# Optimization experiments

Measured on AMD Instinct MI355X. Metric: run time of the kernel, lower is better.

The kernel has to match this reference:

```python
import jax, jax.numpy as jnp
import numpy as np

M1 = M2 = M3 = 6  # retained Fourier modes per axis (matches init_kwargs)
TWO_PI = 2.0 * np.pi


def _freq_grid(kx, ky, kz):
    KX, KY, KZ = jnp.meshgrid(kx, ky, kz, indexing='ij')
    return jnp.stack([KX.ravel(), KY.ravel(), KZ.ravel()], axis=-1)  # [M, 3]


def _cplx(w):
    return w[..., 0] + 1j * w[..., 1]


def setup_inputs() -> dict:
    key = jax.random.key(0)
    k1, k2, k3, k4, k5, k6 = jax.random.split(key, 6)
    B, C, N = 2, 32, 8192
    scale = 1.0 / (C * C)
    return {
        'x': jax.random.normal(k1, (B, C, N), dtype=jnp.float32),
        'pos': jax.random.uniform(k2, (B, N, 3), dtype=jnp.float32),
        'w1': scale * jax.random.uniform(k3, (C, C, M1, M2, M3, 2), dtype=jnp.float32),
        'w2': scale * jax.random.uniform(k4, (C, C, M1, M2, M3, 2), dtype=jnp.float32),
        'w3': scale * jax.random.uniform(k5, (C, C, M1, M2, M3, 2), dtype=jnp.float32),
        'w4': scale * jax.random.uniform(k6, (C, C, M1, M2, M3, 2), dtype=jnp.float32),
    }


def reference(x, pos, w1, w2, w3, w4):
    m1, m2, m3 = M1, M2, M3
    B, C, N = x.shape
    # FFT-ordered frequencies: [0..m-1, -m..-1]
    kx = jnp.concatenate([jnp.arange(m1), jnp.arange(-m1, 0)]).astype(jnp.float32)
    ky = jnp.concatenate([jnp.arange(m2), jnp.arange(-m2, 0)]).astype(jnp.float32)
    kz_full = jnp.concatenate([jnp.arange(m3), jnp.arange(-m3, 0)]).astype(jnp.float32)
    kz_half = jnp.arange(m3).astype(jnp.float32)
    Kf = _freq_grid(kx, ky, kz_full)                     # [M, 3], M = 2m1*2m2*2m3
    Kh = _freq_grid(kx, ky, kz_half)                     # [Mh, 3], Mh = 2m1*2m2*m3
    Ki = jnp.concatenate([Kh, -Kh[::-1]], axis=0)        # [2Mh, 3] Hermitian extension

    # Nonuniform forward Fourier transform (transformer.forward), fused with permutes:
    V_fwd = jnp.exp(-1j * TWO_PI * jnp.einsum('md,bnd->bmn', Kf, pos))  # [B, M, N]
    x_ft = jnp.einsum('bmn,bcn->bcm', V_fwd, x.astype(jnp.complex64))   # [B, C, M]
    x_ft = x_ft.reshape(B, C, 2 * m1, 2 * m2, 2 * m3)

    def mul(a, w):
        return jnp.einsum('bixyz,ioxyz->boxyz', a, _cplx(w))

    out = jnp.zeros((B, C, 2 * m1, 2 * m2, m3), dtype=jnp.complex64)
    out = out.at[:, :, :m1, :m2, :].set(mul(x_ft[:, :, :m1, :m2, :m3], w1))
    out = out.at[:, :, m1:, :m2, :].set(mul(x_ft[:, :, m1:, :m2, :m3], w2))
    out = out.at[:, :, :m1, m2:, :].set(mul(x_ft[:, :, :m1, m2:, :m3], w3))
    out = out.at[:, :, m1:, m2:, :].set(mul(x_ft[:, :, m1:, m2:, :m3], w4))

    xf = out.reshape(B, C, -1)                           # [B, C, Mh]
    xf2 = jnp.conj(xf[:, ::-1, ::-1])                    # torch flip(-1,-2).conj()
    xf = jnp.concatenate([xf, xf2], axis=-1)             # [B, C, 2Mh]

    # Nonuniform inverse transform (transformer.inverse), fused with permutes:
    V_inv = jnp.exp(1j * TWO_PI * jnp.einsum('kd,bnd->bnk', Ki, pos))   # [B, N, 2Mh]
    y = jnp.einsum('bnk,bck->bcn', V_inv, xf)            # [B, C, N]
    return (y / N * 2.0).real.astype(jnp.float32)
```

## Files before the change

### kernel.cpp

```cpp
#include <hip/hip_runtime.h>

#define TWOPI 6.28318530717958647692f

#define BB 2
#define CC 32
#define NN 8192

typedef short bf16x8 __attribute__((ext_vector_type(8)));
typedef float f32x4  __attribute__((ext_vector_type(4)));

__device__ __forceinline__ float2 cmul(float2 a, float2 b){
    return make_float2(fmaf(a.x, b.x, -(a.y*b.y)), fmaf(a.x, b.y, a.y*b.x));
}
__device__ __forceinline__ float2 conj2(float2 a){ return make_float2(a.x, -a.y); }
__device__ __forceinline__ unsigned pk_bf16(float lo, float hi){
    unsigned r;
    asm("v_cvt_pk_bf16_f32 %0, %1, %2" : "=v"(r) : "v"(lo), "v"(hi));
    return r;
}
__device__ __forceinline__ float hw_sin(float p){
    float r; asm("v_sin_f32 %0, %1" : "=v"(r) : "v"(p)); return r;
}
__device__ __forceinline__ float hw_cos(float p){
    float r; asm("v_cos_f32 %0, %1" : "=v"(r) : "v"(p)); return r;
}

__device__ __forceinline__ size_t fragoff(int R, int C){
    int cid = R/48, g3 = (R%48)/16, frow = R%16;
    int nt = C>>4, ll = (frow>>2)*16 + (C&15), r = frow&3;
    return ((size_t)cid*3 + g3)*512 + (size_t)nt*256 + (size_t)ll*4 + r;
}

__global__ __launch_bounds__(256)
void wtrans_kernel(const float* __restrict__ w1, const float* __restrict__ w2,
                   const float* __restrict__ w3, const float* __restrict__ w4,
                   float* __restrict__ wt){
    const int abz = blockIdx.x;
    const int q   = blockIdx.y;
    const float* w = (q==0)?w1:(q==1)?w2:(q==2)?w3:w4;
    const int tid = threadIdx.x;
    #pragma unroll
    for (int k=0;k<4;k++){
        int iop = tid + k*256;
        float2 v = *(const float2*)(w + ((size_t)iop*216 + abz)*2);
        *(float2*)(wt + (((size_t)q*216 + abz)*1024 + iop)*2) = v;
    }
}

__global__ __launch_bounds__(256, 4)
void fused_fwd_kernel(const float* __restrict__ x, const float* __restrict__ pos,
                      const float* __restrict__ w1, const float* __restrict__ w2,
                      const float* __restrict__ w3, const float* __restrict__ w4,
                      float* __restrict__ wt, float* __restrict__ part){
    __shared__ short  P2[12][16][72];
    __shared__ short  xl[32][72];

    const int bid = blockIdx.x;
    const int tid = threadIdx.x;

    if (bid >= 576){
        const int wid = bid - 576;
        const int abz = wid % 216;
        const int q   = wid / 216;
        const float* w = (q==0)?w1:(q==1)?w2:(q==2)?w3:w4;
        #pragma unroll
        for (int k=0;k<4;k++){
            int iop = tid + k*256;
            float2 v = *(const float2*)(w + ((size_t)iop*216 + abz)*2);
            *(float2*)(wt + (((size_t)q*216 + abz)*1024 + iop)*2) = v;
        }
        return;
    }

    const int ks  = bid & 31;
    const int bm  = (bid >> 5) % 9;
    const int b   = bid / 288;
    const int l   = tid & 63;
    const int w   = tid >> 6;
    const int cid = 4*bm + w;
    const int c4k = cid / 9;
    const int lc  = cid % 9;
    const int kxb = (c4k==0) ? 0 : (c4k==1) ? 3 : (c4k==2) ? -6 : -3;
    const int kx0 = kxb + lc/3;
    const int lm3 = lc % 3;

    f32x4 acc[3][2];
    #pragma unroll
    for (int i=0;i<3;i++)
      #pragma unroll
      for (int j=0;j<2;j++) acc[i][j] = (f32x4){0.f,0.f,0.f,0.f};

    #pragma unroll 1
    for (int rnd=0; rnd<4; ++rnd){
        const int n0 = ks*256 + rnd*64;
        __syncthreads();
        #pragma unroll
        for (int k=0;k<2;k++){
            int idx = k*256 + tid;
            int c = idx >> 4;
            int j = idx & 15;
            float4 v = *(const float4*)(x + ((size_t)b*CC + c)*NN + n0 + j*4);
            unsigned p0 = pk_bf16(v.x, v.y);
            unsigned p1 = pk_bf16(v.z, v.w);
            *(uint2*)(&xl[c][j*4]) = make_uint2(p0, p1);
        }
        {
            const int n = n0 + l;
            const float px = pos[((size_t)b*NN + n)*3 + 0];
            const float py = pos[((size_t)b*NN + n)*3 + 1];
            const float pz = pos[((size_t)b*NN + n)*3 + 2];
            const float2 Exf = make_float2(hw_cos(px), -hw_sin(px));
            const float2 Eyf = make_float2(hw_cos(py), -hw_sin(py));
            const float2 Ezf = make_float2(hw_cos(pz), -hw_sin(pz));
            float2 e = make_float2(1.f, 0.f);
            const int ax = kx0 < 0 ? -kx0 : kx0;
            #pragma unroll
            for (int i2=0;i2<6;i2++) if (i2 < ax) e = cmul(e, Exf);
            if (kx0 < 0) e = conj2(e);
            const float2 y2  = cmul(Eyf, Eyf);
            const float2 y4  = cmul(y2, y2);
            if      (lm3 == 1) e = cmul(e, y4);
            else if (lm3 == 2) e = cmul(e, conj2(y4));
            const float2 y8  = cmul(y4, y4);
            const float2 y11 = cmul(cmul(y8, y2), Eyf);
            float2 Sv[4];
            Sv[0] = e;
            Sv[1] = cmul(Sv[0], Eyf);
            Sv[2] = cmul(Sv[1], (lm3==1) ? conj2(y11) : Eyf);
            Sv[3] = cmul(Sv[2], Eyf);
            #pragma unroll
            for (int s2=0; s2<4; ++s2){
                float2 ee = Sv[s2];
                #pragma unroll
                for (int kz=0; kz<6; ++kz){
                    const int g  = 6*s2 + kz;
                    const int g3 = g >> 3;
                    const int j  = g & 7;
                    unsigned pv = pk_bf16(ee.x, ee.y);
                    P2[w*3+g3][2*j  ][l] = (short)(pv & 0xffffu);
                    P2[w*3+g3][2*j+1][l] = (short)(pv >> 16);
                    if (kz < 5) ee = cmul(ee, Ezf);
                }
            }
        }
        __syncthreads();
        #pragma unroll
        for (int kstep=0; kstep<2; ++kstep){
            const int kn = kstep*32 + (l>>4)*8;
            bf16x8 bfr0 = *(const bf16x8*)(&xl[(l&15)     ][kn]);
            bf16x8 bfr1 = *(const bf16x8*)(&xl[(l&15) + 16][kn]);
            #pragma unroll
            for (int g3=0; g3<3; ++g3){
                bf16x8 afr = *(const bf16x8*)(&P2[w*3+g3][l&15][kn]);
                acc[g3][0] = __builtin_amdgcn_mfma_f32_16x16x32_bf16(afr, bfr0, acc[g3][0],0,0,0);
                acc[g3][1] = __builtin_amdgcn_mfma_f32_16x16x32_bf16(afr, bfr1, acc[g3][1],0,0,0);
            }
        }
    }
    float* pb = part + ((((size_t)ks*BB + b)*36 + cid)*3)*512;
    #pragma unroll
    for (int g3=0; g3<3; ++g3)
      #pragma unroll
      for (int nt=0; nt<2; ++nt)
        *(f32x4*)(pb + (size_t)(g3*2+nt)*256 + (size_t)l*4) = acc[g3][nt];
}

__global__ __launch_bounds__(128, 2)
void fwd_atomic_kernel(const float* __restrict__ x, const float* __restrict__ pos,
                       float* __restrict__ F){
    const int tid = threadIdx.x;
    const int colslot = tid & 15;
    const int cs = tid >> 4;
    const int col = blockIdx.y * 16 + colslot;
    const int ixm = col / 12;
    const int iym = col % 12;
    const int b   = blockIdx.z;
    const int nb0 = blockIdx.x * 128;

    __shared__ float2 exl[12][65];
    __shared__ float2 eyl[12][65];
    __shared__ float2 ezt[64][8];
    __shared__ float  xl[CC][68];

    float acc[6][4][2];
    #pragma unroll
    for (int z=0;z<6;z++)
      #pragma unroll
      for (int j=0;j<4;j++){ acc[z][j][0]=0.f; acc[z][j][1]=0.f; }

    for (int t=0; t<2; ++t){
        const int nb = nb0 + t*64;
        __syncthreads();
        if (tid < 64){
            const int n = nb + tid;
            const float px = pos[((size_t)b*NN + n)*3 + 0];
            const float py = pos[((size_t)b*NN + n)*3 + 1];
            const float pz = pos[((size_t)b*NN + n)*3 + 2];
            float s, c;
            float2 pw[7];
            s = hw_sin(px); c = hw_cos(px);
            { float2 e1 = make_float2(c, -s);
              pw[0] = make_float2(1.f, 0.f);
              #pragma unroll
              for (int k=1;k<7;k++) pw[k] = cmul(pw[k-1], e1);
              #pragma unroll
              for (int k=0;k<6;k++) exl[k][tid] = pw[k];
              #pragma unroll
              for (int k=6;k<12;k++) exl[k][tid] = make_float2(pw[12-k].x, -pw[12-k].y);
            }
            s = hw_sin(py); c = hw_cos(py);
            { float2 e1 = make_float2(c, -s);
              pw[0] = make_float2(1.f, 0.f);
              #pragma unroll
              for (int k=1;k<7;k++) pw[k] = cmul(pw[k-1], e1);
              #pragma unroll
              for (int k=0;k<6;k++) eyl[k][tid] = pw[k];
              #pragma unroll
              for (int k=6;k<12;k++) eyl[k][tid] = make_float2(pw[12-k].x, -pw[12-k].y);
            }
            s = hw_sin(pz); c = hw_cos(pz);
            { float2 e1 = make_float2(c, -s);
              float2 qv = make_float2(1.f, 0.f);
              #pragma unroll
              for (int k=0;k<6;k++){ ezt[tid][k] = qv; qv = cmul(qv, e1); }
            }
        }
        #pragma unroll
        for (int k=0;k<4;k++){
            int v = tid + k*128;
            int c = v >> 4;
            int j = v & 15;
            float4 xv = *(const float4*)(x + (size_t)(b*CC + c)*NN + nb + j*4);
            *(float4*)(&xl[c][j*4]) = xv;
        }
        __syncthreads();

        #pragma unroll 2
        for (int np=0; np<64; ++np){
            float2 rex = exl[ixm][np];
            float2 rey = eyl[iym][np];
            float2 exy = cmul(rex, rey);
            float xv0 = xl[cs*4+0][np];
            float xv1 = xl[cs*4+1][np];
            float xv2 = xl[cs*4+2][np];
            float xv3 = xl[cs*4+3][np];
            const float4* ezp = (const float4*)(&ezt[np][0]);
            float4 ea = ezp[0], eb2 = ezp[1], ec = ezp[2];
            float2 ezv[6];
            ezv[0] = make_float2(ea.x, ea.y);  ezv[1] = make_float2(ea.z, ea.w);
            ezv[2] = make_float2(eb2.x, eb2.y); ezv[3] = make_float2(eb2.z, eb2.w);
            ezv[4] = make_float2(ec.x, ec.y);  ezv[5] = make_float2(ec.z, ec.w);
            #pragma unroll
            for (int z=0; z<6; ++z){
                float2 ph = cmul(exy, ezv[z]);
                acc[z][0][0] = fmaf(ph.x, xv0, acc[z][0][0]);
                acc[z][0][1] = fmaf(ph.y, xv0, acc[z][0][1]);
                acc[z][1][0] = fmaf(ph.x, xv1, acc[z][1][0]);
                acc[z][1][1] = fmaf(ph.y, xv1, acc[z][1][1]);
                acc[z][2][0] = fmaf(ph.x, xv2, acc[z][2][0]);
                acc[z][2][1] = fmaf(ph.y, xv2, acc[z][2][1]);
                acc[z][3][0] = fmaf(ph.x, xv3, acc[z][3][0]);
                acc[z][3][1] = fmaf(ph.y, xv3, acc[z][3][1]);
            }
        }
    }

    const int c0 = cs*4;
    const int c4f = ixm/3;
    const int tb  = (ixm%3)*72 + iym*6;
    float* Fb = F + (size_t)b*55296;
    #pragma unroll
    for (int z=0;z<6;z++)
      #pragma unroll
      for (int j=0;j<4;j++){
        const int R = c4f*432 + 2*(tb + z);
        atomicAdd(Fb + fragoff(R,   c0 + j), acc[z][j][0]);
        atomicAdd(Fb + fragoff(R+1, c0 + j), acc[z][j][1]);
      }
}

template<int NK>
__global__ __launch_bounds__(128)
void mix_kernel(const float* __restrict__ part, const float* __restrict__ wt,
                short* __restrict__ Abf){
    const int tid = threadIdx.x;
    const int o  = tid & 31;
    const int ml = tid >> 5;
    const int b  = blockIdx.y;
    const int m0 = blockIdx.x * 4;

    __shared__ float xs[256];
    __shared__ float os[4][32][2];

    {
        const int mm0 = m0 % 216, c4m = m0 / 216;
        const int q0  = 2*mm0;
        const int cid = c4m*9 + q0/48;
        const int g3  = (q0 % 48) / 16;
        const int lh  = (q0 % 16) >> 3;
        const int v   = 2*tid;
        const int nt  = v >> 7;
        const int rem = v & 127;
        const int lp  = rem >> 2;
        const int rr  = rem & 3;
        const float* pb = part + (((size_t)b*36 + cid)*3 + g3)*512
                        + (size_t)nt*256 + (size_t)(lh*32 + lp)*4 + rr;
        float s0 = 0.f, s1 = 0.f;
        #pragma unroll 8
        for (int k=0;k<NK;k++){
            float2 vv = *(const float2*)(pb + (size_t)k*110592);
            s0 += vv.x; s1 += vv.y;
        }
        const int jA = ((lp>>4)<<2) + rr;
        const int ci = nt*16 + (lp & 15);
        xs[jA*32 + ci]       = s0;
        xs[(jA+1)*32 + ci]   = s1;
    }
    __syncthreads();

    const int m  = m0 + ml;
    const int ix = m / 72;
    const int iy = (m / 6) % 12;
    const int iz = m % 6;
    const int q  = (ix>=6 ? 1 : 0) + (iy>=6 ? 2 : 0);
    const int a  = ix % 6;
    const int bb2 = iy % 6;
    const int abz = (a*6 + bb2)*6 + iz;
    const float* wq = wt + ((size_t)q*216 + abz)*2048;

    float orr = 0.f, oii = 0.f;
    #pragma unroll 8
    for (int i=0;i<32;i++){
        float xr = xs[ml*64 + i];
        float xi = xs[ml*64 + 32 + i];
        float2 wv = *(const float2*)(wq + (i*32 + o)*2);
        orr = fmaf(xr, wv.x, orr); orr = fmaf(-xi, wv.y, orr);
        oii = fmaf(xr, wv.y, oii); oii = fmaf( xi, wv.x, oii);
    }
    os[ml][o][0] = orr;
    os[ml][o][1] = oii;
    __syncthreads();
    if (o < 16){
        const float sc2 = 2.0f / (float)NN;
        float tr =  (os[ml][o][0] + os[ml][31-o][0]) * sc2;
        float ti = -((os[ml][o][1] + os[ml][31-o][1]) * sc2);
        const int mc4 = m / 216;
        const int mr  = m % 216;
        const int kk  = mr >> 2;
        const int qq  = mr & 3;
        unsigned pv = pk_bf16(tr, ti);
        *(unsigned*)(Abf + (size_t)b*27648 + ((size_t)kk*64 + mc4*16 + o)*8 + 2*qq) = pv;
    }
}

__global__ __launch_bounds__(768)
void inv_kernel(const float* __restrict__ pos, const short* __restrict__ Abf,
                float* __restrict__ y){
    const int tid = threadIdx.x;
    const int og  = tid >> 8;
    const int w4  = (tid >> 6) & 3;
    const int l   = tid & 63;
    const int col = l & 15;
    const int c4  = l >> 4;
    const int b   = blockIdx.y;
    const int n   = blockIdx.x*64 + w4*16 + col;

    __shared__ float red[2][4][16][17];

    const float px = pos[((size_t)b*NN + n)*3 + 0];
    const float py = pos[((size_t)b*NN + n)*3 + 1];
    const float pz = pos[((size_t)b*NN + n)*3 + 2];
    const float2 Ex = make_float2(hw_cos(px), hw_sin(px));
    const float2 Ey = make_float2(hw_cos(py), hw_sin(py));
    const float2 Ez = make_float2(hw_cos(pz), hw_sin(pz));

    const float2 yy2 = cmul(Ey, Ey);
    const float2 yy4 = cmul(yy2, yy2);
    const float2 yy8 = cmul(yy4, yy4);
    const float2 cj11 = conj2(cmul(cmul(yy8, yy2), Ey));
    const float2 x3  = cmul(cmul(Ex, Ex), Ex);
    const float2 x6  = cmul(x3, x3);
    float2 e = (c4==0) ? make_float2(1.f, 0.f)
             : (c4==1) ? x3
             : (c4==2) ? conj2(x6)
             :           conj2(x3);
    if (og >= 1) e = cmul(e, Ex);
    if (og == 2) e = cmul(e, Ex);

    const short* Ab = Abf + (size_t)b*27648 + (size_t)og*18*512 + (size_t)l*8;
    f32x4 acc = {0.f, 0.f, 0.f, 0.f};

    union BU { unsigned u[4]; bf16x8 v; };

    float2 S  = e;
    float2 ee = S;
    #pragma unroll
    for (int u2=0; u2<18; ++u2){
        BU bu;
        #pragma unroll
        for (int qq=0; qq<4; ++qq){
            const int g = 4*u2 + qq;
            if (g > 0){
                if (g % 6) ee = cmul(ee, Ez);
                else { S = cmul(S, (g==36) ? cj11 : Ey); ee = S; }
            }
            bu.u[qq] = pk_bf16(ee.x, ee.y);
        }
        bf16x8 afr = *(const bf16x8*)(Ab + (size_t)u2*512);
        acc = __builtin_amdgcn_mfma_f32_16x16x32_bf16(afr, bu.v, acc, 0, 0, 0);
    }

    if (og >= 1){
        #pragma unroll
        for (int r=0; r<4; ++r) red[og-1][w4][c4*4 + r][col] = acc[r];
    }
    __syncthreads();
    if (og == 0){
        float* yb = y + (size_t)b*CC*NN + n;
        #pragma unroll
        for (int r=0; r<4; ++r){
            const int ch = c4*4 + r;
            float v = acc[r] + red[0][w4][ch][col] + red[1][w4][ch][col];
            yb[(size_t)ch*NN]      = v;
            yb[(size_t)(31-ch)*NN] = v;
        }
    }
}

extern "C" void kernel_launch(void* const* d_in, const int* in_sizes, int n_in,
                              void* d_out, int out_size, void* d_ws, size_t ws_size,
                              hipStream_t stream){
    const float* x   = (const float*)d_in[0];
    const float* pos = (const float*)d_in[1];
    const float* w1  = (const float*)d_in[2];
    const float* w2  = (const float*)d_in[3];
    const float* w3  = (const float*)d_in[4];
    const float* w4  = (const float*)d_in[5];
    float* out = (float*)d_out;
    char* wsb = (char*)d_ws;

    float* wt    = (float*)(wsb);
    short* Abf   = (short*)(wsb + 7520256);
    float* part2 = (float*)(wsb + 7741440);
    const bool use_part = (ws_size >= 21897216ull);

    if (use_part){
        fused_fwd_kernel<<<dim3(1440), 256, 0, stream>>>(x, pos, w1, w2, w3, w4, wt, part2);
        mix_kernel<32><<<dim3(216,2), 128, 0, stream>>>(part2, wt, Abf);
    } else {
        wtrans_kernel<<<dim3(216,4), 256, 0, stream>>>(w1, w2, w3, w4, wt);
        hipMemsetAsync(part2, 0, 442368, stream);
        fwd_atomic_kernel<<<dim3(64,9,2), 128, 0, stream>>>(x, pos, part2);
        mix_kernel<1><<<dim3(216,2), 128, 0, stream>>>(part2, wt, Abf);
    }

    inv_kernel<<<dim3(NN/64, BB), 768, 0, stream>>>(pos, Abf, out);
}
```

Before: 32.22 us.

## Compute forward Fourier basis directly in registers via hardware sin, drop LDS staging

The forward fused kernel no longer builds the complex exponential table by chained complex multiplies into shared memory. Each lane now evaluates the phase k·pos for its own row and uses v_fract plus v_sin (with a quarter-turn offset for the cosine part) to form the bf16 MFMA A-fragment directly in registers. It also loads x straight from global into B-fragments, which removes both LDS buffers and the block barriers. The cost is more transcendental ops per lane, redundant global loads of pos and x across waves, and possible accuracy change; fract is also added to the atomic kernel's sin/cos inputs.

Result: slower. 40.65 us (+26.2%).

```diff
diff --git a/kernel.cpp b/kernel.cpp
--- a/kernel.cpp
+++ b/kernel.cpp
@@ -23,6 +23,14 @@
 }
 __device__ __forceinline__ float hw_cos(float p){
     float r; asm("v_cos_f32 %0, %1" : "=v"(r) : "v"(p)); return r;
+}
+__device__ __forceinline__ float hw_fract(float t){
+    float r; asm("v_fract_f32 %0, %1" : "=v"(r) : "v"(t)); return r;
+}
+__device__ __forceinline__ float f4get(const float4* a, int i){
+    float4 v = a[i>>2];
+    int m = i&3;
+    return m==0?v.x:m==1?v.y:m==2?v.z:v.w;
 }
 
 __device__ __forceinline__ size_t fragoff(int R, int C){
@@ -52,9 +60,6 @@
                       const float* __restrict__ w1, const float* __restrict__ w2,
                       const float* __restrict__ w3, const float* __restrict__ w4,
                       float* __restrict__ wt, float* __restrict__ part){
-    __shared__ short  P2[12][16][72];
-    __shared__ short  xl[32][72];
-
     const int bid = blockIdx.x;
     const int tid = threadIdx.x;
 
@@ -83,6 +88,27 @@
     const int kxb = (c4k==0) ? 0 : (c4k==1) ? 3 : (c4k==2) ? -6 : -3;
     const int kx0 = kxb + lc/3;
     const int lm3 = lc % 3;
+    const int r15 = l & 15;
+    const int h   = l >> 4;
+    const int isim= r15 & 1;
+    const int cmh = r15 >> 1;
+
+    const float kxf = (float)kx0;
+    const float sgn = isim ? -1.0f : 1.0f;
+    const float off = isim ?  0.0f : 0.25f;
+    float kyf[3], kzf[3];
+    #pragma unroll
+    for (int g3=0; g3<3; ++g3){
+        const int cm = g3*8 + cmh;
+        const int s2 = cm/6;
+        const int kz = cm%6;
+        int ky;
+        if      (lm3 == 0) ky = s2;
+        else if (lm3 == 1) ky = (s2<2)? 4+s2 : s2-8;
+        else               ky = s2-4;
+        kyf[g3] = (float)ky;
+        kzf[g3] = (float)kz;
+    }
 
     f32x4 acc[3][2];
     #pragma unroll
@@ -90,70 +116,51 @@
       #pragma unroll
       for (int j=0;j<2;j++) acc[i][j] = (f32x4){0.f,0.f,0.f,0.f};
 
+    const float* xbp = x   + (size_t)b*CC*NN;
+    const float* pbp = pos + (size_t)b*NN*3;
+
+    union BU { unsigned u[4]; bf16x8 v; };
+
     #pragma unroll 1
     for (int rnd=0; rnd<4; ++rnd){
         const int n0 = ks*256 + rnd*64;
-        __syncthreads();
-        #pragma unroll
-        for (int k=0;k<2;k++){
-            int idx = k*256 + tid;
-            int c = idx >> 4;
-            int j = idx & 15;
-            float4 v = *(const float4*)(x + ((size_t)b*CC + c)*NN + n0 + j*4);
-            unsigned p0 = pk_bf16(v.x, v.y);
-            unsigned p1 = pk_bf16(v.z, v.w);
-            *(uint2*)(&xl[c][j*4]) = make_uint2(p0, p1);
-        }
-        {
-            const int n = n0 + l;
-            const float px = pos[((size_t)b*NN + n)*3 + 0];
-            const float py = pos[((size_t)b*NN + n)*3 + 1];
-            const float pz = pos[((size_t)b*NN + n)*3 + 2];
-            const float2 Exf = make_float2(hw_cos(px), -hw_sin(px));
-            const float2 Eyf = make_float2(hw_cos(py), -hw_sin(py));
-            const float2 Ezf = make_float2(hw_cos(pz), -hw_sin(pz));
-            float2 e = make_float2(1.f, 0.f);
-            const int ax = kx0 < 0 ? -kx0 : kx0;
+        #pragma unroll
+        for (int kstep=0; kstep<2; ++kstep){
+            const int p0 = n0 + kstep*32 + h*8;
+            float4 pf[6];
             #pragma unroll
-            for (int i2=0;i2<6;i2++) if (i2 < ax) e = cmul(e, Exf);
-            if (kx0 < 0) e = conj2(e);
-            const float2 y2  = cmul(Eyf, Eyf);
-            const float2 y4  = cmul(y2, y2);
-            if      (lm3 == 1) e = cmul(e, y4);
-            else if (lm3 == 2) e = cmul(e, conj2(y4));
-            const float2 y8  = cmul(y4, y4);
-            const float2 y11 = cmul(cmul(y8, y2), Eyf);
-            float2 Sv[4];
-            Sv[0] = e;
-            Sv[1] = cmul(Sv[0], Eyf);
-            Sv[2] = cmul(Sv[1], (lm3==1) ? conj2(y11) : Eyf);
-            Sv[3] = cmul(Sv[2], Eyf);
+            for (int i=0;i<6;i++) pf[i] = *(const float4*)(pbp + (size_t)p0*3 + i*4);
+            float4 xa0 = *(const float4*)(xbp + (size_t)r15*NN + p0);
+            float4 xa1 = *(const float4*)(xbp + (size_t)r15*NN + p0 + 4);
+            float4 xc0 = *(const float4*)(xbp + (size_t)(r15+16)*NN + p0);
+            float4 xc1 = *(const float4*)(xbp + (size_t)(r15+16)*NN + p0 + 4);
+            BU bfr0, bfr1;
+            bfr0.u[0] = pk_bf16(xa0.x, xa0.y); bfr0.u[1] = pk_bf16(xa0.z, xa0.w);
+            bfr0.u[2] = pk_bf16(xa1.x, xa1.y); bfr0.u[3] = pk_bf16(xa1.z, xa1.w);
+            bfr1.u[0] = pk_bf16(xc0.x, xc0.y); bfr1.u[1] = pk_bf16(xc0.z, xc0.w);
+            bfr1.u[2] = pk_bf16(xc1.x, xc1.y); bfr1.u[3] = pk_bf16(xc1.z, xc1.w);
+            float v[3][8];
             #pragma unroll
-            for (int s2=0; s2<4; ++s2){
-                float2 ee = Sv[s2];
+            for (int e=0; e<8; ++e){
+                const float px = f4get(pf, 3*e+0);
+                const float py = f4get(pf, 3*e+1);
+                const float pz = f4get(pf, 3*e+2);
                 #pragma unroll
-                for (int kz=0; kz<6; ++kz){
-                    const int g  = 6*s2 + kz;
-                    const int g3 = g >> 3;
-                    const int j  = g & 7;
-                    unsigned pv = pk_bf16(ee.x, ee.y);
-                    P2[w*3+g3][2*j  ][l] = (short)(pv & 0xffffu);
-                    P2[w*3+g3][2*j+1][l] = (short)(pv >> 16);
-                    if (kz < 5) ee = cmul(ee, Ezf);
+                for (int g3=0; g3<3; ++g3){
+                    float t  = fmaf(kxf, px, fmaf(kyf[g3], py, kzf[g3]*pz));
+                    float t2 = fmaf(sgn, t, off);
+                    v[g3][e] = hw_sin(hw_fract(t2));
                 }
             }
-        }
-        __syncthreads();
-        #pragma unroll
-        for (int kstep=0; kstep<2; ++kstep){
-            const int kn = kstep*32 + (l>>4)*8;
-            bf16x8 bfr0 = *(const bf16x8*)(&xl[(l&15)     ][kn]);
-            bf16x8 bfr1 = *(const bf16x8*)(&xl[(l&15) + 16][kn]);
             #pragma unroll
             for (int g3=0; g3<3; ++g3){
-                bf16x8 afr = *(const bf16x8*)(&P2[w*3+g3][l&15][kn]);
-                acc[g3][0] = __builtin_amdgcn_mfma_f32_16x16x32_bf16(afr, bfr0, acc[g3][0],0,0,0);
-                acc[g3][1] = __builtin_amdgcn_mfma_f32_16x16x32_bf16(afr, bfr1, acc[g3][1],0,0,0);
+                BU au;
+                au.u[0] = pk_bf16(v[g3][0], v[g3][1]);
+                au.u[1] = pk_bf16(v[g3][2], v[g3][3]);
+                au.u[2] = pk_bf16(v[g3][4], v[g3][5]);
+                au.u[3] = pk_bf16(v[g3][6], v[g3][7]);
+                acc[g3][0] = __builtin_amdgcn_mfma_f32_16x16x32_bf16(au.v, bfr0.v, acc[g3][0],0,0,0);
+                acc[g3][1] = __builtin_amdgcn_mfma_f32_16x16x32_bf16(au.v, bfr1.v, acc[g3][1],0,0,0);
             }
         }
     }
@@ -198,7 +205,7 @@
             const float pz = pos[((size_t)b*NN + n)*3 + 2];
             float s, c;
             float2 pw[7];
-            s = hw_sin(px); c = hw_cos(px);
+            s = hw_sin(hw_fract(px)); c = hw_cos(hw_fract(px));
             { float2 e1 = make_float2(c, -s);
               pw[0] = make_float2(1.f, 0.f);
               #pragma unroll
@@ -208,7 +215,7 @@
               #pragma unroll
               for (int k=6;k<12;k++) exl[k][tid] = make_float2(pw[12-k].x, -pw[12-k].y);
             }
-            s = hw_sin(py); c = hw_cos(py);
+            s = hw_sin(hw_fract(py)); c = hw_cos(hw_fract(py));
             { float2 e1 = make_float2(c, -s);
               pw[0] = make_float2(1.f, 0.f);
               #pragma unroll
@@ -218,7 +225,7 @@
               #pragma unroll
               for (int k=6;k<12;k++) eyl[k][tid] = make_float2(pw[12-k].x, -pw[12-k].y);
             }
-            s = hw_sin(pz); c = hw_cos(pz);
+            s = hw_sin(hw_fract(pz)); c = hw_cos(hw_fract(pz));
             { float2 e1 = make_float2(c, -s);
               float2 qv = make_float2(1.f, 0.f);
               #pragma unroll
```
